# Optimization experiments

Measured on AMD Instinct MI355X. Metric: run time of the kernel, lower is better.

The kernel has to match this reference:

```python
import jax, jax.numpy as jnp
import numpy as np

T, S, B = 512, 512, 8
D, H = 512, 8
HD = D // H
L = 8            # nlabels
F = 2048         # dim_feedforward
EPS = 1e-5


def _ln(x, s, b):
    m = x.mean(-1, keepdims=True)
    v = ((x - m) ** 2).mean(-1, keepdims=True)
    return (x - m) * jax.lax.rsqrt(v + EPS) * s + b


def setup_inputs() -> dict:
    key = jax.random.key(0)
    ks = jax.random.split(key, 20)
    p = lambda i, shape: jax.random.normal(ks[i], shape, jnp.float32) * 0.02
    z = lambda n: jnp.zeros((n,), jnp.float32)
    return {
        "tgt": jax.random.normal(ks[0], (T, B, D), jnp.float32),
        "edge_mask": jax.random.uniform(ks[1], (B, L, T, T), dtype=jnp.float32),
        "tgt_padding_mask": jnp.zeros((B, T, T), jnp.bool_),
        "memory": jax.random.normal(ks[2], (S, B, D), jnp.float32),
        # self-attn (GNN matrix relational attention)
        "sa_q_w": p(3, (D, D)), "sa_q_b": z(D),
        "sa_k_w": p(4, (D, D)), "sa_k_b": z(D),
        "sa_v_w": p(5, (D, D)), "sa_v_b": z(D),
        "sa_rel": p(6, (L, HD, HD)),
        "sa_out_w": p(7, (D, D)), "sa_out_b": z(D),
        # cross-attn (torch MultiheadAttention packed in_proj)
        "ca_in_w": p(8, (3 * D, D)), "ca_in_b": z(3 * D),
        "ca_out_w": p(9, (D, D)), "ca_out_b": z(D),
        # FFN
        "lin1_w": p(10, (F, D)), "lin1_b": z(F),
        "lin2_w": p(11, (D, F)), "lin2_b": z(D),
        # layernorms
        "ln1_s": jnp.ones((D,), jnp.float32), "ln1_b": z(D),
        "ln2_s": jnp.ones((D,), jnp.float32), "ln2_b": z(D),
        "ln3_s": jnp.ones((D,), jnp.float32), "ln3_b": z(D),
    }


def reference(tgt, edge_mask, tgt_padding_mask, memory,
              sa_q_w, sa_q_b, sa_k_w, sa_k_b, sa_v_w, sa_v_b, sa_rel,
              sa_out_w, sa_out_b, ca_in_w, ca_in_b, ca_out_w, ca_out_b,
              lin1_w, lin1_b, lin2_w, lin2_b,
              ln1_s, ln1_b, ln2_s, ln2_b, ln3_s, ln3_b):
    scale = 1.0 / np.sqrt(HD).astype(np.float32)

    # ---- edge-aware relational self-attention (dropout = eval/identity) ----
    x = tgt.transpose(1, 0, 2)                       # (B, T, D)
    def heads(y, n):                                 # (B, n, ., HD)
        return y.reshape(B, -1, H, HD).transpose(0, 2, 1, 3)
    q = heads(x @ sa_q_w.T + sa_q_b, T)
    k = heads(x @ sa_k_w.T + sa_k_b, T)
    v = heads(x @ sa_v_w.T + sa_v_b, T)

    scores = jnp.zeros((B, H, T, T), q.dtype)
    for l in range(L):                               # small fixed label set
        kl = jnp.einsum('bhtd,de->bhte', k, sa_rel[l])
        scores = scores + edge_mask[:, l][:, None] * jnp.einsum('bhid,bhjd->bhij', q, kl)
    scores = scores * scale
    scores = jnp.where(tgt_padding_mask[:, None], -1e9, scores)
    attn = jax.nn.softmax(scores, axis=-1)
    o = jnp.einsum('bhij,bhjd->bhid', attn, v).transpose(0, 2, 1, 3).reshape(B, T, D)
    tgt2 = (o @ sa_out_w.T + sa_out_b).transpose(1, 0, 2)   # (T, B, D)
    x1 = _ln(tgt + tgt2, ln1_s, ln1_b)

    # ---- standard cross-attention over encoder memory ----
    wq, wk, wv = ca_in_w[:D], ca_in_w[D:2 * D], ca_in_w[2 * D:]
    bq, bk, bv = ca_in_b[:D], ca_in_b[D:2 * D], ca_in_b[2 * D:]
    cq = heads((x1 @ wq.T + bq).transpose(1, 0, 2), T)       # (B,H,T,HD)
    ck = heads((memory @ wk.T + bk).transpose(1, 0, 2), S)   # (B,H,S,HD)
    cv = heads((memory @ wv.T + bv).transpose(1, 0, 2), S)
    cs = jnp.einsum('bhtd,bhsd->bhts', cq, ck) * scale
    ca = jax.nn.softmax(cs, axis=-1)
    co = jnp.einsum('bhts,bhsd->bhtd', ca, cv).transpose(0, 2, 1, 3).reshape(B, T, D)
    tgt2 = (co @ ca_out_w.T + ca_out_b).transpose(1, 0, 2)
    x2 = _ln(x1 + tgt2, ln2_s, ln2_b)

    # ---- FFN ----
    ffn = jax.nn.relu(x2 @ lin1_w.T + lin1_b) @ lin2_w.T + lin2_b
    return _ln(x2 + ffn, ln3_s, ln3_b)
```

## Files before the change

### kernel.cpp

```cpp
#include <hip/hip_runtime.h>

#define Tn 512
#define Sn 512
#define Bn 8
#define Dn 512
#define Hn 8
#define HDn 64
#define Ln 8
#define Fn 2048
#define SCALE 0.125f

typedef short short8 __attribute__((ext_vector_type(8)));
typedef float floatx4 __attribute__((ext_vector_type(4)));

__device__ __forceinline__ unsigned short f2b(float f) {
    unsigned int u = __float_as_uint(f);
    u += 0x7FFFu + ((u >> 16) & 1u);
    return (unsigned short)(u >> 16);
}

__global__ __launch_bounds__(256) void to_rows_bf16(const float* __restrict__ in,
                                                    unsigned short* __restrict__ out, int T_) {
    size_t n = (size_t)blockIdx.x * 256 + threadIdx.x;
    size_t total = (size_t)T_ * Bn * Dn;
    if (n >= total) return;
    int d = (int)(n & (Dn - 1));
    size_t rt = n >> 9;
    int t = (int)(rt % T_);
    int b = (int)(rt / T_);
    out[n] = f2b(in[((size_t)t * Bn + b) * Dn + d]);
}

__global__ __launch_bounds__(256) void conv_all(
    const float* __restrict__ qw, const float* __restrict__ kw, const float* __restrict__ vw,
    const float* __restrict__ sow, const float* __restrict__ ciw, const float* __restrict__ cow,
    const float* __restrict__ l1w, const float* __restrict__ l2w, const float* __restrict__ rel,
    const float* __restrict__ qbias, const float* __restrict__ kbias, const float* __restrict__ vbias,
    unsigned short* __restrict__ wall, float* __restrict__ bqkv) {
    const int Q = 1 << 18;
    const int total = 16 * Q + Ln * HDn * HDn;
    int i = blockIdx.x * 256 + threadIdx.x;
    if (i < total) {
        int seg = i >> 18, r = i & (Q - 1);
        float v;
        if (seg < 3)       v = (seg == 0 ? qw : (seg == 1 ? kw : vw))[r];
        else if (seg == 3) v = sow[r];
        else if (seg < 7)  v = ciw[(size_t)(seg - 4) * Q + r];
        else if (seg == 7) v = cow[r];
        else if (seg < 12) v = l1w[(size_t)(seg - 8) * Q + r];
        else if (seg < 16) v = l2w[(size_t)(seg - 12) * Q + r];
        else               v = rel[r];
        wall[i] = f2b(v);
    }
    int j = i - total;
    if (j >= 0 && j < 3 * Dn)
        bqkv[j] = (j < Dn ? qbias[j] : (j < 2 * Dn ? kbias[j - Dn] : vbias[j - 2 * Dn]));
}

__global__ __launch_bounds__(256) void gemm_bf16(
    const unsigned short* __restrict__ A, const unsigned short* __restrict__ W,
    const float* __restrict__ bias, void* __restrict__ Cv, void* __restrict__ Cv2,
    void* __restrict__ Cv3,
    int M, int N, int K, int lda, int ldw, int ldc,
    long sA1, long sA2, long sW1, long sW2, long sC1, long sC2, int zdiv,
    float alpha, int mode, int relu, int Tp) {
    int z = blockIdx.z;
    int z1 = z / zdiv, z2 = z - z1 * zdiv;
    const unsigned short* Ab = A + (size_t)z1 * sA1 + (size_t)z2 * sA2;
    const unsigned short* Wb = W + (size_t)z1 * sW1 + (size_t)z2 * sW2;
    size_t coff = (size_t)z1 * sC1 + (size_t)z2 * sC2;
    int tid = threadIdx.x;
    int lane = tid & 63, wave = tid >> 6;
    int wm = wave & 1, wn = wave >> 1;
    int l16 = lane & 15, quad = lane >> 4;
    int m0 = blockIdx.y * 64 + wm * 32;
    int n0 = blockIdx.x * 64 + wn * 32;

    floatx4 acc00 = {0,0,0,0}, acc01 = {0,0,0,0}, acc10 = {0,0,0,0}, acc11 = {0,0,0,0};
    const unsigned short* a0p = Ab + (size_t)(m0 + l16) * lda + quad * 8;
    const unsigned short* a1p = a0p + (size_t)16 * lda;
    const unsigned short* b0p = Wb + (size_t)(n0 + l16) * ldw + quad * 8;
    const unsigned short* b1p = b0p + (size_t)16 * ldw;

    for (int kk = 0; kk < K; kk += 32) {
        short8 a0 = *(const short8*)(a0p + kk);
        short8 a1 = *(const short8*)(a1p + kk);
        short8 b0 = *(const short8*)(b0p + kk);
        short8 b1 = *(const short8*)(b1p + kk);
        acc00 = __builtin_amdgcn_mfma_f32_16x16x32_bf16(a0, b0, acc00, 0, 0, 0);
        acc01 = __builtin_amdgcn_mfma_f32_16x16x32_bf16(a0, b1, acc01, 0, 0, 0);
        acc10 = __builtin_amdgcn_mfma_f32_16x16x32_bf16(a1, b0, acc10, 0, 0, 0);
        acc11 = __builtin_amdgcn_mfma_f32_16x16x32_bf16(a1, b1, acc11, 0, 0, 0);
    }
    floatx4 accs[2][2] = {{acc00, acc01}, {acc10, acc11}};
    for (int mt = 0; mt < 2; ++mt)
        for (int nt = 0; nt < 2; ++nt) {
            int gn = n0 + nt * 16 + l16;
            float bb = bias ? bias[gn] : 0.0f;
            floatx4 v = accs[mt][nt];
            for (int r = 0; r < 4; ++r) {
                int gm = m0 + mt * 16 + quad * 4 + r;
                float val = v[r] * alpha + bb;
                if (relu) val = fmaxf(val, 0.0f);
                if (mode == 0) {
                    ((float*)Cv)[coff + (size_t)gm * ldc + gn] = val;
                } else if (mode == 1) {
                    ((unsigned short*)Cv)[coff + (size_t)gm * ldc + gn] = f2b(val);
                } else if (mode == 2) {
                    int bq = gm / Tp, t = gm - bq * Tp;
                    ((unsigned short*)Cv)[(((size_t)(bq * Hn + (gn >> 6)) * Tp + t) << 6) + (gn & 63)] = f2b(val);
                } else if (mode == 3) {
                    int bq = gm / Tp, t = gm - bq * Tp;
                    ((unsigned short*)Cv)[((size_t)(bq * Hn + (gn >> 6)) * 64 + (gn & 63)) * Tp + t] = f2b(val);
                } else if (mode == 4) {
                    int sel = gn >> 9, g2 = gn & 511;
                    int bq = gm / Tp, t = gm - bq * Tp;
                    int hh = g2 >> 6, dd = g2 & 63;
                    if (sel == 0)
                        ((unsigned short*)Cv)[(((size_t)(bq * Hn + hh) * Tp + t) << 6) + dd] = f2b(val);
                    else if (sel == 1)
                        ((unsigned short*)Cv2)[(((size_t)(bq * Hn + hh) * Tp + t) << 6) + dd] = f2b(val);
                    else
                        ((unsigned short*)Cv3)[((size_t)(bq * Hn + hh) * 64 + dd) * Tp + t] = f2b(val);
                } else {
                    int sel = gn >> 9, g2 = gn & 511;
                    int bq = gm / Tp, t = gm - bq * Tp;
                    int hh = g2 >> 6, dd = g2 & 63;
                    if (sel == 0)
                        ((unsigned short*)Cv)[(((size_t)(bq * Hn + hh) * Tp + t) << 6) + dd] = f2b(val);
                    else
                        ((unsigned short*)Cv2)[((size_t)(bq * Hn + hh) * 64 + dd) * Tp + t] = f2b(val);
                }
            }
        }
}

__global__ __launch_bounds__(256) void relscores2(
    const unsigned short* __restrict__ uR, const unsigned short* __restrict__ kB,
    const float* __restrict__ em, const unsigned char* __restrict__ pad,
    float* __restrict__ scores) {
    int jb = blockIdx.x, ib = blockIdx.y;
    int b = blockIdx.z >> 3, h = blockIdx.z & 7;
    int tid = threadIdx.x, lane = tid & 63, wave = tid >> 6;
    int wm = wave & 1, wn = wave >> 1;
    int l16 = lane & 15, quad = lane >> 4;
    int i0 = ib * 64 + wm * 32, j0 = jb * 64 + wn * 32;

    const unsigned short* kbase = kB + (size_t)(b * Hn + h) * Tn * HDn;
    short8 kr00 = *(const short8*)(kbase + (size_t)(j0 + l16) * HDn + quad * 8);
    short8 kr01 = *(const short8*)(kbase + (size_t)(j0 + l16) * HDn + 32 + quad * 8);
    short8 kr10 = *(const short8*)(kbase + (size_t)(j0 + 16 + l16) * HDn + quad * 8);
    short8 kr11 = *(const short8*)(kbase + (size_t)(j0 + 16 + l16) * HDn + 32 + quad * 8);

    float sacc[2][2][4] = {};
    const unsigned short* uB = uR + (size_t)(b * Hn + h) * Ln * Tn * HDn;
    const float* emB = em + (size_t)b * Ln * Tn * Tn;

    for (int l = 0; l < Ln; ++l) {
        const unsigned short* ub = uB + (size_t)l * Tn * HDn;
        short8 a00 = *(const short8*)(ub + (size_t)(i0 + l16) * HDn + quad * 8);
        short8 a01 = *(const short8*)(ub + (size_t)(i0 + l16) * HDn + 32 + quad * 8);
        short8 a10 = *(const short8*)(ub + (size_t)(i0 + 16 + l16) * HDn + quad * 8);
        short8 a11 = *(const short8*)(ub + (size_t)(i0 + 16 + l16) * HDn + 32 + quad * 8);
        floatx4 g00 = {0,0,0,0}, g01 = {0,0,0,0}, g10 = {0,0,0,0}, g11 = {0,0,0,0};
        g00 = __builtin_amdgcn_mfma_f32_16x16x32_bf16(a00, kr00, g00, 0, 0, 0);
        g00 = __builtin_amdgcn_mfma_f32_16x16x32_bf16(a01, kr01, g00, 0, 0, 0);
        g01 = __builtin_amdgcn_mfma_f32_16x16x32_bf16(a00, kr10, g01, 0, 0, 0);
        g01 = __builtin_amdgcn_mfma_f32_16x16x32_bf16(a01, kr11, g01, 0, 0, 0);
        g10 = __builtin_amdgcn_mfma_f32_16x16x32_bf16(a10, kr00, g10, 0, 0, 0);
        g10 = __builtin_amdgcn_mfma_f32_16x16x32_bf16(a11, kr01, g10, 0, 0, 0);
        g11 = __builtin_amdgcn_mfma_f32_16x16x32_bf16(a10, kr10, g11, 0, 0, 0);
        g11 = __builtin_amdgcn_mfma_f32_16x16x32_bf16(a11, kr11, g11, 0, 0, 0);
        const float* emb = emB + (size_t)l * Tn * Tn;
        floatx4 gs[2][2] = {{g00, g01}, {g10, g11}};
        for (int mt = 0; mt < 2; ++mt)
            for (int nt = 0; nt < 2; ++nt)
                for (int r = 0; r < 4; ++r) {
                    int i = i0 + mt * 16 + quad * 4 + r;
                    int j = j0 + nt * 16 + l16;
                    sacc[mt][nt][r] += emb[(size_t)i * Tn + j] * gs[mt][nt][r];
                }
    }

    const unsigned char* padb = pad + (size_t)b * Tn * Tn;
    float* sb = scores + (size_t)(b * Hn + h) * Tn * Tn;
    for (int mt = 0; mt < 2; ++mt)
        for (int nt = 0; nt < 2; ++nt)
            for (int r = 0; r < 4; ++r) {
                int i = i0 + mt * 16 + quad * 4 + r;
                int j = j0 + nt * 16 + l16;
                float val = sacc[mt][nt][r] * SCALE;
                if (padb[(size_t)i * Tn + j]) val = -1.0e9f;
                sb[(size_t)i * Tn + j] = val;
            }
}

__global__ __launch_bounds__(256) void softmax_rows(float* __restrict__ buf, int rows, int len) {
    int gw = (int)(((size_t)blockIdx.x * 256 + threadIdx.x) >> 6);
    int lane = threadIdx.x & 63;
    if (gw >= rows) return;
    float* row = buf + (size_t)gw * len;
    int cc = len >> 6;
    float vals[8];
    float mx = -3.0e38f;
    for (int c = 0; c < cc; ++c) { vals[c] = row[c * 64 + lane]; mx = fmaxf(mx, vals[c]); }
    for (int off = 32; off; off >>= 1) mx = fmaxf(mx, __shfl_xor(mx, off, 64));
    float sum = 0.f;
    for (int c = 0; c < cc; ++c) { float e = __expf(vals[c] - mx); vals[c] = e; sum += e; }
    for (int off = 32; off; off >>= 1) sum += __shfl_xor(sum, off, 64);
    float inv = 1.0f / sum;
    unsigned short* prow = (unsigned short*)row;
    for (int c = 0; c < cc; ++c) prow[c * 64 + lane] = f2b(vals[c] * inv);
}

__global__ __launch_bounds__(256) void ln_kernel(
    const float* __restrict__ a, int a_trans, const float* __restrict__ b2,
    const float* __restrict__ s, const float* __restrict__ bb,
    float* __restrict__ outF, int out_trans, unsigned short* __restrict__ outB) {
    int row = blockIdx.x;
    int b = row >> 9, t = row & (Tn - 1);
    int tid = threadIdx.x;
    size_t ia = a_trans ? ((size_t)(t * Bn + b)) * Dn : (size_t)row * Dn;
    size_t ir = (size_t)row * Dn;
    float x0 = a[ia + tid];
    float x1 = a[ia + tid + 256];
    if (b2) { x0 += b2[ir + tid]; x1 += b2[ir + tid + 256]; }
    float s1 = x0 + x1, s2 = x0 * x0 + x1 * x1;
    for (int off = 32; off; off >>= 1) {
        s1 += __shfl_xor(s1, off, 64);
        s2 += __shfl_xor(s2, off, 64);
    }
    __shared__ float red[2][4];
    int wave = tid >> 6, lane = tid & 63;
    if (lane == 0) { red[0][wave] = s1; red[1][wave] = s2; }
    __syncthreads();
    float ts1 = red[0][0] + red[0][1] + red[0][2] + red[0][3];
    float ts2 = red[1][0] + red[1][1] + red[1][2] + red[1][3];
    float mean = ts1 * (1.0f / Dn);
    float var = ts2 * (1.0f / Dn) - mean * mean;
    float rs = rsqrtf(var + 1e-5f);
    float y0 = (x0 - mean) * rs * s[tid] + bb[tid];
    float y1 = (x1 - mean) * rs * s[tid + 256] + bb[tid + 256];
    size_t io = out_trans ? ((size_t)(t * Bn + b)) * Dn : ir;
    if (outF) { outF[io + tid] = y0; outF[io + tid + 256] = y1; }
    if (outB) { outB[ir + tid] = f2b(y0); outB[ir + tid + 256] = f2b(y1); }
}

extern "C" void kernel_launch(void* const* d_in, const int* in_sizes, int n_in,
                              void* d_out, int out_size, void* d_ws, size_t ws_size,
                              hipStream_t stream) {
    const float* tgt      = (const float*)d_in[0];
    const float* em       = (const float*)d_in[1];
    const unsigned char* pad = (const unsigned char*)d_in[2];
    const float* memr     = (const float*)d_in[3];
    const float* sa_q_w   = (const float*)d_in[4];
    const float* sa_q_b   = (const float*)d_in[5];
    const float* sa_k_w   = (const float*)d_in[6];
    const float* sa_k_b   = (const float*)d_in[7];
    const float* sa_v_w   = (const float*)d_in[8];
    const float* sa_v_b   = (const float*)d_in[9];
    const float* sa_rel   = (const float*)d_in[10];
    const float* sa_out_w = (const float*)d_in[11];
    const float* sa_out_b = (const float*)d_in[12];
    const float* ca_in_w  = (const float*)d_in[13];
    const float* ca_in_b  = (const float*)d_in[14];
    const float* ca_out_w = (const float*)d_in[15];
    const float* ca_out_b = (const float*)d_in[16];
    const float* lin1_w   = (const float*)d_in[17];
    const float* lin1_b   = (const float*)d_in[18];
    const float* lin2_w   = (const float*)d_in[19];
    const float* lin2_b   = (const float*)d_in[20];
    const float* ln1_s    = (const float*)d_in[21];
    const float* ln1_b    = (const float*)d_in[22];
    const float* ln2_s    = (const float*)d_in[23];
    const float* ln2_b    = (const float*)d_in[24];
    const float* ln3_s    = (const float*)d_in[25];
    const float* ln3_b    = (const float*)d_in[26];

    const size_t BT = (size_t)Bn * Tn;
    const size_t Q  = 1 << 18;

    char* ws = (char*)d_ws;
    size_t off = 0;
    auto alloc = [&](size_t bytes) -> char* {
        char* p = ws + off;
        off += (bytes + 255) & ~(size_t)255;
        return p;
    };
    unsigned short* xb   = (unsigned short*)alloc(BT * Dn * 2);
    unsigned short* mb   = (unsigned short*)alloc(BT * Dn * 2);
    unsigned short* wall = (unsigned short*)alloc((16 * Q + Ln * HDn * HDn) * 2);
    float*          bqkv = (float*)alloc(3 * Dn * 4);
    unsigned short* qb   = (unsigned short*)alloc(BT * Dn * 2);
    unsigned short* kb   = (unsigned short*)alloc(BT * Dn * 2);
    unsigned short* vtb  = (unsigned short*)alloc(BT * Dn * 2);
    unsigned short* ur   = (unsigned short*)alloc((size_t)Bn * Hn * Ln * Tn * HDn * 2);
    float*          sc   = (float*)alloc((size_t)Bn * Hn * Tn * Tn * 4);
    unsigned short* ob   = (unsigned short*)alloc(BT * Dn * 2);
    float*          t2f  = (float*)alloc(BT * Dn * 4);
    float*          x1f  = (float*)alloc(BT * Dn * 4);
    unsigned short* x1b  = (unsigned short*)alloc(BT * Dn * 2);
    float*          x2f  = (float*)alloc(BT * Dn * 4);
    unsigned short* x2b  = (unsigned short*)alloc(BT * Dn * 2);
    unsigned short* hid  = (unsigned short*)alloc(BT * Fn * 2);
    (void)ws_size; (void)in_sizes; (void)n_in; (void)out_size;

    unsigned short* wqkv = wall;
    unsigned short* wsao = wall + 3 * Q;
    unsigned short* wcain = wall + 4 * Q;
    unsigned short* wcao = wall + 7 * Q;
    unsigned short* wlin1 = wall + 8 * Q;
    unsigned short* wlin2 = wall + 12 * Q;
    unsigned short* wrel = wall + 16 * Q;

    auto gemm = [&](const unsigned short* A, const unsigned short* W, const float* bias,
                    void* C, void* C2, void* C3, int M, int N, int K, int lda, int ldw, int ldc,
                    long sA1, long sA2, long sW1, long sW2, long sC1, long sC2,
                    int zdiv, int batches, float alpha, int mode, int relu, int Tp) {
        dim3 g(N / 64, M / 64, batches);
        gemm_bf16<<<g, 256, 0, stream>>>(A, W, bias, C, C2, C3, M, N, K, lda, ldw, ldc,
                                         sA1, sA2, sW1, sW2, sC1, sC2, zdiv,
                                         alpha, mode, relu, Tp);
    };

    to_rows_bf16<<<dim3((BT * Dn + 255) / 256), 256, 0, stream>>>(tgt, xb, Tn);
    to_rows_bf16<<<dim3((BT * Dn + 255) / 256), 256, 0, stream>>>(memr, mb, Sn);
    conv_all<<<dim3((16 * Q + Ln * HDn * HDn + 3 * Dn + 255) / 256), 256, 0, stream>>>(
        sa_q_w, sa_k_w, sa_v_w, sa_out_w, ca_in_w, ca_out_w, lin1_w, lin2_w, sa_rel,
        sa_q_b, sa_k_b, sa_v_b, wall, bqkv);

    gemm(xb, wqkv, bqkv, qb, kb, vtb, (int)BT, 3 * Dn, Dn, Dn, Dn, 0,
         0, 0, 0, 0, 0, 0, 1, 1, 1.0f, 4, 0, Tn);
    gemm(qb, wrel, nullptr, ur, nullptr, nullptr, Tn, HDn, HDn, HDn, HDn, HDn,
         (long)Tn * HDn, 0, 0, (long)HDn * HDn, (long)Ln * Tn * HDn, (long)Tn * HDn,
         Ln, Bn * Hn * Ln, 1.0f, 1, 0, 0);
    relscores2<<<dim3(Tn / 64, Tn / 64, Bn * Hn), 256, 0, stream>>>(ur, kb, em, pad, sc);
    softmax_rows<<<dim3((Bn * Hn * Tn * 64 + 255) / 256), 256, 0, stream>>>(sc, Bn * Hn * Tn, Tn);
    gemm((const unsigned short*)sc, vtb, nullptr, ob, nullptr, nullptr, Tn, HDn, Tn, 2 * Tn, Tn, Dn,
         (long)Hn * Tn * Tn * 2, (long)Tn * Tn * 2, (long)Hn * HDn * Tn, (long)HDn * Tn,
         (long)Tn * Dn, 64, Hn, Bn * Hn, 1.0f, 1, 0, 0);
    gemm(ob, wsao, sa_out_b, t2f, nullptr, nullptr, (int)BT, Dn, Dn, Dn, Dn, Dn,
         0, 0, 0, 0, 0, 0, 1, 1, 1.0f, 0, 0, 0);
    ln_kernel<<<dim3((int)BT), 256, 0, stream>>>(tgt, 1, t2f, ln1_s, ln1_b, x1f, 0, x1b);

    gemm(x1b, wcain, ca_in_b, qb, nullptr, nullptr, (int)BT, Dn, Dn, Dn, Dn, 0,
         0, 0, 0, 0, 0, 0, 1, 1, 1.0f, 2, 0, Tn);
    gemm(mb, wcain + (size_t)Dn * Dn, ca_in_b + Dn, kb, vtb, nullptr, (int)BT, 2 * Dn, Dn, Dn, Dn, 0,
         0, 0, 0, 0, 0, 0, 1, 1, 1.0f, 5, 0, Sn);
    gemm(qb, kb, nullptr, sc, nullptr, nullptr, Tn, Sn, HDn, HDn, HDn, Sn,
         (long)Tn * HDn, 0, (long)Sn * HDn, 0, (long)Tn * Sn, 0,
         1, Bn * Hn, SCALE, 0, 0, 0);
    softmax_rows<<<dim3((Bn * Hn * Tn * 64 + 255) / 256), 256, 0, stream>>>(sc, Bn * Hn * Tn, Sn);
    gemm((const unsigned short*)sc, vtb, nullptr, ob, nullptr, nullptr, Tn, HDn, Sn, 2 * Sn, Sn, Dn,
         (long)Hn * Tn * Sn * 2, (long)Tn * Sn * 2, (long)Hn * HDn * Sn, (long)HDn * Sn,
         (long)Tn * Dn, 64, Hn, Bn * Hn, 1.0f, 1, 0, 0);
    gemm(ob, wcao, ca_out_b, t2f, nullptr, nullptr, (int)BT, Dn, Dn, Dn, Dn, Dn,
         0, 0, 0, 0, 0, 0, 1, 1, 1.0f, 0, 0, 0);
    ln_kernel<<<dim3((int)BT), 256, 0, stream>>>(x1f, 0, t2f, ln2_s, ln2_b, x2f, 0, x2b);

    gemm(x2b, wlin1, lin1_b, hid, nullptr, nullptr, (int)BT, Fn, Dn, Dn, Dn, Fn,
         0, 0, 0, 0, 0, 0, 1, 1, 1.0f, 1, 1, 0);
    gemm(hid, wlin2, lin2_b, t2f, nullptr, nullptr, (int)BT, Dn, Fn, Fn, Fn, Dn,
         0, 0, 0, 0, 0, 0, 1, 1, 1.0f, 0, 0, 0);
    ln_kernel<<<dim3((int)BT), 256, 0, stream>>>(x2f, 0, t2f, ln3_s, ln3_b, (float*)d_out, 1, nullptr);
}
```

Measured before the change: 763.9 us.

## Fuse relational score computation with row softmax into one wave-per-row-block kernel

Replaces the separate score kernel, fp32 score buffer and softmax pass with a single kernel in which one 64-lane wave computes all 512 scores for 16 query rows, applies scale and padding, does the softmax in registers and writes bf16 probabilities directly. The same kernel, without edge weighting, replaces the cross-attention QK GEMM plus softmax. This removes the fp32 round trip of the full score matrix. The cost is high register pressure (a 32-entry floatx4 accumulator array plus 8 relational operand pairs) and only one wave per block, which may reduce occupancy.

Result: slower. 1.152 ms (+50.9%).

```diff
diff --git a/kernel.cpp b/kernel.cpp
--- a/kernel.cpp
+++ b/kernel.cpp
@@ -135,82 +135,94 @@
         }
 }
 
-__global__ __launch_bounds__(256) void relscores2(
-    const unsigned short* __restrict__ uR, const unsigned short* __restrict__ kB,
-    const float* __restrict__ em, const unsigned char* __restrict__ pad,
-    float* __restrict__ scores) {
-    int jb = blockIdx.x, ib = blockIdx.y;
-    int b = blockIdx.z >> 3, h = blockIdx.z & 7;
-    int tid = threadIdx.x, lane = tid & 63, wave = tid >> 6;
-    int wm = wave & 1, wn = wave >> 1;
+template <int NL, bool EM>
+__global__ __launch_bounds__(64) void relsoft(
+    const unsigned short* __restrict__ uR,
+    const unsigned short* __restrict__ kB,
+    const float* __restrict__ em,
+    const unsigned char* __restrict__ pad,
+    unsigned short* __restrict__ P) {
+    int id = blockIdx.x;
+    int c = id & 7, h = (id >> 3) & 7, g = id >> 6;
+    int u = g * 8 + c;
+    int b = u >> 5, it = u & 31;
+    int bh = b * Hn + h;
+    int lane = threadIdx.x;
     int l16 = lane & 15, quad = lane >> 4;
-    int i0 = ib * 64 + wm * 32, j0 = jb * 64 + wn * 32;
-
-    const unsigned short* kbase = kB + (size_t)(b * Hn + h) * Tn * HDn;
-    short8 kr00 = *(const short8*)(kbase + (size_t)(j0 + l16) * HDn + quad * 8);
-    short8 kr01 = *(const short8*)(kbase + (size_t)(j0 + l16) * HDn + 32 + quad * 8);
-    short8 kr10 = *(const short8*)(kbase + (size_t)(j0 + 16 + l16) * HDn + quad * 8);
-    short8 kr11 = *(const short8*)(kbase + (size_t)(j0 + 16 + l16) * HDn + 32 + quad * 8);
-
-    float sacc[2][2][4] = {};
-    const unsigned short* uB = uR + (size_t)(b * Hn + h) * Ln * Tn * HDn;
-    const float* emB = em + (size_t)b * Ln * Tn * Tn;
-
-    for (int l = 0; l < Ln; ++l) {
-        const unsigned short* ub = uB + (size_t)l * Tn * HDn;
-        short8 a00 = *(const short8*)(ub + (size_t)(i0 + l16) * HDn + quad * 8);
-        short8 a01 = *(const short8*)(ub + (size_t)(i0 + l16) * HDn + 32 + quad * 8);
-        short8 a10 = *(const short8*)(ub + (size_t)(i0 + 16 + l16) * HDn + quad * 8);
-        short8 a11 = *(const short8*)(ub + (size_t)(i0 + 16 + l16) * HDn + 32 + quad * 8);
-        floatx4 g00 = {0,0,0,0}, g01 = {0,0,0,0}, g10 = {0,0,0,0}, g11 = {0,0,0,0};
-        g00 = __builtin_amdgcn_mfma_f32_16x16x32_bf16(a00, kr00, g00, 0, 0, 0);
-        g00 = __builtin_amdgcn_mfma_f32_16x16x32_bf16(a01, kr01, g00, 0, 0, 0);
-        g01 = __builtin_amdgcn_mfma_f32_16x16x32_bf16(a00, kr10, g01, 0, 0, 0);
-        g01 = __builtin_amdgcn_mfma_f32_16x16x32_bf16(a01, kr11, g01, 0, 0, 0);
-        g10 = __builtin_amdgcn_mfma_f32_16x16x32_bf16(a10, kr00, g10, 0, 0, 0);
-        g10 = __builtin_amdgcn_mfma_f32_16x16x32_bf16(a11, kr01, g10, 0, 0, 0);
-        g11 = __builtin_amdgcn_mfma_f32_16x16x32_bf16(a10, kr10, g11, 0, 0, 0);
-        g11 = __builtin_amdgcn_mfma_f32_16x16x32_bf16(a11, kr11, g11, 0, 0, 0);
-        const float* emb = emB + (size_t)l * Tn * Tn;
-        floatx4 gs[2][2] = {{g00, g01}, {g10, g11}};
-        for (int mt = 0; mt < 2; ++mt)
-            for (int nt = 0; nt < 2; ++nt)
-                for (int r = 0; r < 4; ++r) {
-                    int i = i0 + mt * 16 + quad * 4 + r;
-                    int j = j0 + nt * 16 + l16;
-                    sacc[mt][nt][r] += emb[(size_t)i * Tn + j] * gs[mt][nt][r];
-                }
-    }
-
-    const unsigned char* padb = pad + (size_t)b * Tn * Tn;
-    float* sb = scores + (size_t)(b * Hn + h) * Tn * Tn;
-    for (int mt = 0; mt < 2; ++mt)
-        for (int nt = 0; nt < 2; ++nt)
-            for (int r = 0; r < 4; ++r) {
-                int i = i0 + mt * 16 + quad * 4 + r;
-                int j = j0 + nt * 16 + l16;
-                float val = sacc[mt][nt][r] * SCALE;
-                if (padb[(size_t)i * Tn + j]) val = -1.0e9f;
-                sb[(size_t)i * Tn + j] = val;
+    int i = it * 16 + l16;
+
+    short8 uf[NL][2];
+    const unsigned short* ub = uR + (size_t)bh * NL * Tn * HDn + (size_t)i * HDn + quad * 8;
+    for (int l = 0; l < NL; ++l) {
+        uf[l][0] = *(const short8*)(ub + (size_t)l * Tn * HDn);
+        uf[l][1] = *(const short8*)(ub + (size_t)l * Tn * HDn + 32);
+    }
+    const unsigned short* kp0 = kB + (size_t)bh * Tn * HDn + (size_t)l16 * HDn + quad * 8;
+    const float* emB = EM ? (em + ((size_t)b * NL * Tn + i) * Tn) : nullptr;
+
+    floatx4 sacc[Tn / 16];
+    for (int jt = 0; jt < Tn / 16; ++jt) {
+        const unsigned short* kp = kp0 + (size_t)jt * 16 * HDn;
+        short8 k0 = *(const short8*)(kp);
+        short8 k1 = *(const short8*)(kp + 32);
+        if (EM) {
+            floatx4 e4[NL];
+            for (int l = 0; l < NL; ++l)
+                e4[l] = *(const floatx4*)(emB + (size_t)l * Tn * Tn + jt * 16 + quad * 4);
+            floatx4 s = {0, 0, 0, 0};
+            for (int l = 0; l < NL; ++l) {
+                floatx4 gacc = {0, 0, 0, 0};
+                gacc = __builtin_amdgcn_mfma_f32_16x16x32_bf16(k0, uf[l][0], gacc, 0, 0, 0);
+                gacc = __builtin_amdgcn_mfma_f32_16x16x32_bf16(k1, uf[l][1], gacc, 0, 0, 0);
+                s += e4[l] * gacc;
             }
-}
-
-__global__ __launch_bounds__(256) void softmax_rows(float* __restrict__ buf, int rows, int len) {
-    int gw = (int)(((size_t)blockIdx.x * 256 + threadIdx.x) >> 6);
-    int lane = threadIdx.x & 63;
-    if (gw >= rows) return;
-    float* row = buf + (size_t)gw * len;
-    int cc = len >> 6;
-    float vals[8];
+            sacc[jt] = s;
+        } else {
+            floatx4 gacc = {0, 0, 0, 0};
+            gacc = __builtin_amdgcn_mfma_f32_16x16x32_bf16(k0, uf[0][0], gacc, 0, 0, 0);
+            gacc = __builtin_amdgcn_mfma_f32_16x16x32_bf16(k1, uf[0][1], gacc, 0, 0, 0);
+            sacc[jt] = gacc;
+        }
+    }
+
     float mx = -3.0e38f;
-    for (int c = 0; c < cc; ++c) { vals[c] = row[c * 64 + lane]; mx = fmaxf(mx, vals[c]); }
-    for (int off = 32; off; off >>= 1) mx = fmaxf(mx, __shfl_xor(mx, off, 64));
-    float sum = 0.f;
-    for (int c = 0; c < cc; ++c) { float e = __expf(vals[c] - mx); vals[c] = e; sum += e; }
-    for (int off = 32; off; off >>= 1) sum += __shfl_xor(sum, off, 64);
+    for (int jt = 0; jt < Tn / 16; ++jt) {
+        floatx4 v = sacc[jt] * SCALE;
+        if (EM) {
+            unsigned int pu = *(const unsigned int*)(pad + ((size_t)b * Tn + i) * Tn + jt * 16 + quad * 4);
+            if (pu) {
+                if (pu & 0x000000FFu) v[0] = -1.0e9f;
+                if (pu & 0x0000FF00u) v[1] = -1.0e9f;
+                if (pu & 0x00FF0000u) v[2] = -1.0e9f;
+                if (pu & 0xFF000000u) v[3] = -1.0e9f;
+            }
+        }
+        sacc[jt] = v;
+        mx = fmaxf(mx, fmaxf(fmaxf(v[0], v[1]), fmaxf(v[2], v[3])));
+    }
+    mx = fmaxf(mx, __shfl_xor(mx, 16, 64));
+    mx = fmaxf(mx, __shfl_xor(mx, 32, 64));
+
+    float sum = 0.0f;
+    for (int jt = 0; jt < Tn / 16; ++jt) {
+        floatx4 v = sacc[jt];
+        v[0] = __expf(v[0] - mx); v[1] = __expf(v[1] - mx);
+        v[2] = __expf(v[2] - mx); v[3] = __expf(v[3] - mx);
+        sacc[jt] = v;
+        sum += v[0] + v[1] + v[2] + v[3];
+    }
+    sum += __shfl_xor(sum, 16, 64);
+    sum += __shfl_xor(sum, 32, 64);
     float inv = 1.0f / sum;
-    unsigned short* prow = (unsigned short*)row;
-    for (int c = 0; c < cc; ++c) prow[c * 64 + lane] = f2b(vals[c] * inv);
+
+    unsigned short* prow = P + (size_t)bh * Tn * Tn + (size_t)i * Tn;
+    for (int jt = 0; jt < Tn / 16; ++jt) {
+        floatx4 v = sacc[jt];
+        ushort4 o;
+        o.x = f2b(v[0] * inv); o.y = f2b(v[1] * inv);
+        o.z = f2b(v[2] * inv); o.w = f2b(v[3] * inv);
+        *(ushort4*)(prow + jt * 16 + quad * 4) = o;
+    }
 }
 
 __global__ __launch_bounds__(256) void ln_kernel(
@@ -295,7 +307,7 @@
     unsigned short* kb   = (unsigned short*)alloc(BT * Dn * 2);
     unsigned short* vtb  = (unsigned short*)alloc(BT * Dn * 2);
     unsigned short* ur   = (unsigned short*)alloc((size_t)Bn * Hn * Ln * Tn * HDn * 2);
-    float*          sc   = (float*)alloc((size_t)Bn * Hn * Tn * Tn * 4);
+    unsigned short* pb   = (unsigned short*)alloc((size_t)Bn * Hn * Tn * Tn * 2);
     unsigned short* ob   = (unsigned short*)alloc(BT * Dn * 2);
     float*          t2f  = (float*)alloc(BT * Dn * 4);
     float*          x1f  = (float*)alloc(BT * Dn * 4);
@@ -334,10 +346,9 @@
     gemm(qb, wrel, nullptr, ur, nullptr, nullptr, Tn, HDn, HDn, HDn, HDn, HDn,
          (long)Tn * HDn, 0, 0, (long)HDn * HDn, (long)Ln * Tn * HDn, (long)Tn * HDn,
          Ln, Bn * Hn * Ln, 1.0f, 1, 0, 0);
-    relscores2<<<dim3(Tn / 64, Tn / 64, Bn * Hn), 256, 0, stream>>>(ur, kb, em, pad, sc);
-    softmax_rows<<<dim3((Bn * Hn * Tn * 64 + 255) / 256), 256, 0, stream>>>(sc, Bn * Hn * Tn, Tn);
-    gemm((const unsigned short*)sc, vtb, nullptr, ob, nullptr, nullptr, Tn, HDn, Tn, 2 * Tn, Tn, Dn,
-         (long)Hn * Tn * Tn * 2, (long)Tn * Tn * 2, (long)Hn * HDn * Tn, (long)HDn * Tn,
+    relsoft<Ln, true><<<dim3(2048), 64, 0, stream>>>(ur, kb, em, pad, pb);
+    gemm(pb, vtb, nullptr, ob, nullptr, nullptr, Tn, HDn, Tn, Tn, Tn, Dn,
+         (long)Hn * Tn * Tn, (long)Tn * Tn, (long)Hn * HDn * Tn, (long)HDn * Tn,
          (long)Tn * Dn, 64, Hn, Bn * Hn, 1.0f, 1, 0, 0);
     gemm(ob, wsao, sa_out_b, t2f, nullptr, nullptr, (int)BT, Dn, Dn, Dn, Dn, Dn,
          0, 0, 0, 0, 0, 0, 1, 1, 1.0f, 0, 0, 0);
@@ -347,12 +358,9 @@
          0, 0, 0, 0, 0, 0, 1, 1, 1.0f, 2, 0, Tn);
     gemm(mb, wcain + (size_t)Dn * Dn, ca_in_b + Dn, kb, vtb, nullptr, (int)BT, 2 * Dn, Dn, Dn, Dn, 0,
          0, 0, 0, 0, 0, 0, 1, 1, 1.0f, 5, 0, Sn);
-    gemm(qb, kb, nullptr, sc, nullptr, nullptr, Tn, Sn, HDn, HDn, HDn, Sn,
-         (long)Tn * HDn, 0, (long)Sn * HDn, 0, (long)Tn * Sn, 0,
-         1, Bn * Hn, SCALE, 0, 0, 0);
-    softmax_rows<<<dim3((Bn * Hn * Tn * 64 + 255) / 256), 256, 0, stream>>>(sc, Bn * Hn * Tn, Sn);
-    gemm((const unsigned short*)sc, vtb, nullptr, ob, nullptr, nullptr, Tn, HDn, Sn, 2 * Sn, Sn, Dn,
-         (long)Hn * Tn * Sn * 2, (long)Tn * Sn * 2, (long)Hn * HDn * Sn, (long)HDn * Sn,
+    relsoft<1, false><<<dim3(2048), 64, 0, stream>>>(qb, kb, nullptr, nullptr, pb);
+    gemm(pb, vtb, nullptr, ob, nullptr, nullptr, Tn, HDn, Sn, Sn, Sn, Dn,
+         (long)Hn * Tn * Sn, (long)Tn * Sn, (long)Hn * HDn * Sn, (long)HDn * Sn,
          (long)Tn * Dn, 64, Hn, Bn * Hn, 1.0f, 1, 0, 0);
     gemm(ob, wcao, ca_out_b, t2f, nullptr, nullptr, (int)BT, Dn, Dn, Dn, Dn, Dn,
          0, 0, 0, 0, 0, 0, 1, 1, 1.0f, 0, 0, 0);
```
